# Kernel tuning notes

Measured on AMD Instinct MI355X. Metric: run time of the kernel, lower is better.

## Reference

```python
import jax, jax.numpy as jnp
import numpy as np

D_MODEL = 1024
NUM_HEAD = 16


def setup_inputs() -> dict:
    key = jax.random.key(0)
    ks = jax.random.split(key, 11)
    B, S, D = 2, 2048, D_MODEL
    scale = 1.0 / np.sqrt(D)
    inp = {
        "Q": jax.random.normal(ks[0], (B, S, D), jnp.float32),
        "K": jax.random.normal(ks[1], (B, S, D), jnp.float32),
        "V": jax.random.normal(ks[2], (B, S, D), jnp.float32),
        "Wq": jax.random.normal(ks[3], (D, D), jnp.float32) * scale,
        "bq": jax.random.normal(ks[4], (D,), jnp.float32) * 0.01,
        "Wk": jax.random.normal(ks[5], (D, D), jnp.float32) * scale,
        "bk": jax.random.normal(ks[6], (D,), jnp.float32) * 0.01,
        "Wv": jax.random.normal(ks[7], (D, D), jnp.float32) * scale,
        "bv": jax.random.normal(ks[8], (D,), jnp.float32) * 0.01,
        "Wo": jax.random.normal(ks[9], (D, D), jnp.float32) * scale,
        "bo": jax.random.normal(ks[10], (D,), jnp.float32) * 0.01,
    }
    return inp


def reference(Q, K, V, Wq, bq, Wk, bk, Wv, bv, Wo, bo):
    b, vc, d_model = Q.shape
    h = NUM_HEAD
    hd = d_model // h
    # projections (torch Linear: x @ W.T + b)
    q = (Q @ Wq.T + bq).reshape(b, vc, h, hd)
    k = (K @ Wk.T + bk).reshape(b, vc, h, hd)
    v = (V @ Wv.T + bv).reshape(b, vc, h, hd)
    # scores [b,h,q,k]
    atten = jnp.einsum('bqhd,bkhd->bhqk', q, k) / np.sqrt(hd).astype(jnp.float32)
    atten = jax.nn.softmax(atten, axis=3)
    # weighted values -> [b,q,h,hd]
    out = jnp.einsum('bhqd,bdhv->bqhv', atten, v).reshape(b, vc, d_model)
    return out @ Wo.T + bo
```

## Files before the change

### kernel.cpp

```cpp
#include <hip/hip_runtime.h>

#define S_LEN 2048
#define DM 1024
#define NH 16
#define HD 64
#define NB 2

typedef unsigned short u16;
typedef __attribute__((ext_vector_type(8))) short s16x8;
typedef __attribute__((ext_vector_type(8))) unsigned short u16x8;
typedef __attribute__((ext_vector_type(4))) float fx4;
typedef __attribute__((ext_vector_type(2))) unsigned u32x2;

__device__ __forceinline__ u16 f2bf(float f) {
  unsigned u = __builtin_bit_cast(unsigned, f);
  return (u16)((u + 0x7FFFu + ((u >> 16) & 1u)) >> 16);
}

__device__ __forceinline__ unsigned cvt_pk_bf16(float a, float b) {
  unsigned r;
  asm("v_cvt_pk_bf16_f32 %0, %1, %2" : "=v"(r) : "v"(a), "v"(b));
  return r;
}

__device__ __forceinline__ void gload16(const void* g, void* l) {
  __builtin_amdgcn_global_load_lds(
      (const __attribute__((address_space(1))) unsigned*)g,
      (__attribute__((address_space(3))) unsigned*)l, 16, 0, 0);
}

__device__ __forceinline__ fx4 mfma16(s16x8 a, s16x8 b, fx4 c) {
  return __builtin_amdgcn_mfma_f32_16x16x32_bf16(a, b, c, 0, 0, 0);
}

__global__ __launch_bounds__(256) void cvt_all_kernel(
    const float* __restrict__ Q, const float* __restrict__ K,
    const float* __restrict__ V, const float* __restrict__ Wq,
    const float* __restrict__ Wk, const float* __restrict__ Wv,
    const float* __restrict__ Wo, u16* __restrict__ Qc, u16* __restrict__ Kc,
    u16* __restrict__ Vc, u16* __restrict__ Wqb, u16* __restrict__ Wkb,
    u16* __restrict__ Wvb, u16* __restrict__ Wob) {
  const int blk = blockIdx.x;
  const float* src;
  u16* dst;
  float scale = 1.0f;
  int off;
  if (blk < 2048)      { src = Q;  dst = Qc;  off = blk; }
  else if (blk < 4096) { src = K;  dst = Kc;  off = blk - 2048; }
  else if (blk < 6144) { src = V;  dst = Vc;  off = blk - 4096; }
  else if (blk < 6656) { src = Wq; dst = Wqb; off = blk - 6144; scale = 0.18033688f; }
  else if (blk < 7168) { src = Wk; dst = Wkb; off = blk - 6656; }
  else if (blk < 7680) { src = Wv; dst = Wvb; off = blk - 7168; }
  else                 { src = Wo; dst = Wob; off = blk - 7680; }
  const int i = (off * 256 + (int)threadIdx.x) * 8;
  fx4 a = *(const fx4*)(src + i);
  fx4 b = *(const fx4*)(src + i + 4);
  u16x8 o;
  o[0] = f2bf(a[0] * scale); o[1] = f2bf(a[1] * scale);
  o[2] = f2bf(a[2] * scale); o[3] = f2bf(a[3] * scale);
  o[4] = f2bf(b[0] * scale); o[5] = f2bf(b[1] * scale);
  o[6] = f2bf(b[2] * scale); o[7] = f2bf(b[3] * scale);
  *(u16x8*)(dst + i) = o;
}

__device__ __forceinline__ void store_out(u16* C, size_t idx, float v) { C[idx] = f2bf(v); }
__device__ __forceinline__ void store_out(float* C, size_t idx, float v) { C[idx] = v; }

template <typename OUT>
__device__ __forceinline__ void gemm_db_body(const u16* __restrict__ A,
                                             const u16* __restrict__ Bt,
                                             const float* __restrict__ bias,
                                             float bscale, OUT* __restrict__ C,
                                             int m0, int n0) {
  __shared__ u16 Al[2][128 * 32];
  __shared__ u16 Bl[2][128 * 32];
  const int tid = threadIdx.x;
  const int wid = tid >> 6, lane = tid & 63;
  const int g = lane >> 4, lr = lane & 15;
  const int wr = wid >> 1, wc = wid & 1;
  const int row0 = tid >> 2, ch = tid & 3;
  const int chx = ch ^ ((row0 >> 1) & 3);

  fx4 acc[4][4] = {};

  auto stage = [&](int buf, int k0) {
    gload16(A + (size_t)(m0 + row0) * 1024 + k0 + chx * 8,
            (char*)Al[buf] + wid * 1024);
    gload16(A + (size_t)(m0 + 64 + row0) * 1024 + k0 + chx * 8,
            (char*)Al[buf] + 4096 + wid * 1024);
    gload16(Bt + (size_t)(n0 + row0) * 1024 + k0 + chx * 8,
            (char*)Bl[buf] + wid * 1024);
    gload16(Bt + (size_t)(n0 + 64 + row0) * 1024 + k0 + chx * 8,
            (char*)Bl[buf] + 4096 + wid * 1024);
  };
  auto compute = [&](int cur) {
    s16x8 a[4], b[4];
#pragma unroll
    for (int m = 0; m < 4; ++m) {
      const int row = wr * 64 + m * 16 + lr;
      a[m] = *(const s16x8*)((char*)Al[cur] + row * 64 + (g ^ ((row >> 1) & 3)) * 16);
    }
#pragma unroll
    for (int n = 0; n < 4; ++n) {
      const int row = wc * 64 + n * 16 + lr;
      b[n] = *(const s16x8*)((char*)Bl[cur] + row * 64 + (g ^ ((row >> 1) & 3)) * 16);
    }
    __builtin_amdgcn_s_setprio(1);
#pragma unroll
    for (int m = 0; m < 4; ++m)
#pragma unroll
      for (int n = 0; n < 4; ++n) acc[m][n] = mfma16(a[m], b[n], acc[m][n]);
    __builtin_amdgcn_s_setprio(0);
  };

  stage(0, 0);
  __syncthreads();

#pragma unroll 1
  for (int t = 0; t < 32; t += 2) {
    stage(1, (t + 1) * 32);
    compute(0);
    __syncthreads();
    if (t + 2 < 32) stage(0, (t + 2) * 32);
    compute(1);
    __syncthreads();
  }

#pragma unroll
  for (int n = 0; n < 4; ++n) {
    const int col = n0 + wc * 64 + n * 16 + lr;
    const float bv = bias[col] * bscale;
#pragma unroll
    for (int m = 0; m < 4; ++m) {
      const int row = m0 + wr * 64 + m * 16 + g * 4;
#pragma unroll
      for (int j = 0; j < 4; ++j)
        store_out(C, (size_t)(row + j) * 1024 + col, acc[m][n][j] + bv);
    }
  }
}

__global__ __launch_bounds__(256, 3) void gemm_qkv_kernel(
    const u16* Qc, const u16* Kc, const u16* Vc, const u16* Wq, const u16* Wk,
    const u16* Wv, const float* bq, const float* bk, const float* bv, u16* q,
    u16* k, u16* v) {
  const int hw = blockIdx.x + (blockIdx.y << 3) + (blockIdx.z << 8);
  const int xcd = hw & 7, j = hw >> 3;
  const int x = j & 7;
  const int p = xcd + ((j >> 3) << 3);
  const int y = p & 31, z = p >> 5;

  const u16* A;
  const u16* B;
  const float* bias;
  u16* C;
  float bs;
  if (z == 0)      { A = Qc; B = Wq; bias = bq; C = q; bs = 0.18033688f; }
  else if (z == 1) { A = Kc; B = Wk; bias = bk; C = k; bs = 1.0f; }
  else             { A = Vc; B = Wv; bias = bv; C = v; bs = 1.0f; }
  gemm_db_body<u16>(A, B, bias, bs, C, y * 128, x * 128);
}

__global__ __launch_bounds__(256, 3) void gemm_out_kernel(const u16* ctx,
                                                          const u16* Wo,
                                                          const float* bo,
                                                          float* out) {
  const int hw = blockIdx.x + (blockIdx.y << 3);
  const int xcd = hw & 7, j = hw >> 3;
  const int x = j & 7;
  const int y = xcd + ((j >> 3) << 3);
  gemm_db_body<float>(ctx, Wo, bo, 1.0f, out, y * 128, x * 128);
}

__global__ __launch_bounds__(256) void transpose_v_kernel(const u16* __restrict__ v,
                                                          u16* __restrict__ vt) {
  const int bh = blockIdx.y;
  const int b = bh >> 4, h = bh & 15;
  const int s0 = blockIdx.x * 32;
  const int d = threadIdx.x & 63;
  const int c = threadIdx.x >> 6;
  const int s = s0 + c * 8;
  const u16* src = v + ((size_t)(b * S_LEN + s)) * DM + h * HD + d;
  u16x8 o;
#pragma unroll
  for (int e = 0; e < 8; ++e) o[e] = src[(size_t)e * DM];
  *(u16x8*)(vt + ((size_t)(bh * 64 + d)) * S_LEN + s) = o;
}

__global__ __launch_bounds__(256, 4) void attn_kernel(const u16* __restrict__ qb,
                                                      const u16* __restrict__ kb,
                                                      const u16* __restrict__ vt,
                                                      u16* __restrict__ ctx) {
  __shared__ u16 Kl[2][64 * 64];
  __shared__ u16 Vl[2][64 * 64];
  __shared__ u16 Pl[4][16 * 64];

  const int tid = threadIdx.x, wid = tid >> 6, lane = tid & 63;
  const int g = lane >> 4, lr = lane & 15;
  const int rswz = (lr & 7) * 8;
  const int pswz = (lr & 7) * 16;
  char* Pb = (char*)&Pl[wid][0];

  const int hw = blockIdx.x;
  const int xcd = hw & 7, slot = hw >> 3;
  const int bh = xcd * 4 + (slot >> 5);
  const int b = bh >> 4, h = bh & 15;
  const int q0 = (slot & 31) * 64;

  const u16* qp = qb + ((size_t)(b * S_LEN + q0 + wid * 16 + lr)) * DM + h * HD;
  s16x8 aq[2];
  aq[0] = *(const s16x8*)(qp + g * 8);
  aq[1] = *(const s16x8*)(qp + 32 + g * 8);

  fx4 accO[4] = {};
  float lrun = 0.f;

  const int srow = tid >> 3, sch = tid & 7;
  const int schx = sch ^ (srow & 7);
  const u16* kbase = kb + ((size_t)b * S_LEN) * DM + h * HD;
  const u16* vtbase = vt + ((size_t)bh * 64) * S_LEN;

#define STAGE(buf, kv)                                                             \
  do {                                                                             \
    gload16(kbase + (size_t)((kv) + srow) * DM + schx * 8,                         \
            (char*)Kl[buf] + wid * 1024);                                          \
    gload16(kbase + (size_t)((kv) + 32 + srow) * DM + schx * 8,                    \
            (char*)Kl[buf] + 4096 + wid * 1024);                                   \
    gload16(vtbase + (size_t)srow * S_LEN + (kv) + schx * 8,                       \
            (char*)Vl[buf] + wid * 1024);                                          \
    gload16(vtbase + (size_t)(32 + srow) * S_LEN + (kv) + schx * 8,                \
            (char*)Vl[buf] + 4096 + wid * 1024);                                   \
  } while (0)

  auto compute_tile = [&](const u16* Kc0, const u16* Vc0) {
    fx4 s[4] = {};
    __builtin_amdgcn_s_setprio(1);
#pragma unroll
    for (int ks = 0; ks < 2; ++ks) {
#pragma unroll
      for (int c = 0; c < 4; ++c) {
        s16x8 kf =
            *(const s16x8*)(Kc0 + (c * 16 + lr) * 64 + ((ks * 32 + g * 8) ^ rswz));
        s[c] = mfma16(kf, aq[ks], s[c]);
      }
    }
    __builtin_amdgcn_s_setprio(0);

#pragma unroll
    for (int c = 0; c < 4; ++c)
#pragma unroll
      for (int j = 0; j < 4; ++j) s[c][j] = __builtin_amdgcn_exp2f(s[c][j]);
    {
      const float r0 = (s[0][0] + s[0][1]) + (s[0][2] + s[0][3]);
      const float r1 = (s[1][0] + s[1][1]) + (s[1][2] + s[1][3]);
      const float r2 = (s[2][0] + s[2][1]) + (s[2][2] + s[2][3]);
      const float r3 = (s[3][0] + s[3][1]) + (s[3][2] + s[3][3]);
      lrun += (r0 + r1) + (r2 + r3);
    }

#pragma unroll
    for (int c = 0; c < 4; ++c) {
      u32x2 w;
      w[0] = cvt_pk_bf16(s[c][0], s[c][1]);
      w[1] = cvt_pk_bf16(s[c][2], s[c][3]);
      *(u32x2*)(Pb + lr * 128 + ((c * 32 + g * 8) ^ pswz)) = w;
    }

    __builtin_amdgcn_s_setprio(1);
#pragma unroll
    for (int ks = 0; ks < 2; ++ks) {
      s16x8 pb = *(const s16x8*)(Pb + lr * 128 + ((ks * 64 + g * 16) ^ pswz));
#pragma unroll
      for (int c = 0; c < 4; ++c) {
        s16x8 vf =
            *(const s16x8*)(Vc0 + (c * 16 + lr) * 64 + ((ks * 32 + g * 8) ^ rswz));
        accO[c] = mfma16(vf, pb, accO[c]);
      }
    }
    __builtin_amdgcn_s_setprio(0);
  };

  STAGE(0, 0);
  __syncthreads();

  for (int t = 0; t < 32; t += 2) {
    if (t + 1 < 32) STAGE(1, (t + 1) * 64);
    compute_tile(Kl[0], Vl[0]);
    __syncthreads();
    if (t + 2 < 32) STAGE(0, (t + 2) * 64);
    compute_tile(Kl[1], Vl[1]);
    __syncthreads();
  }
#undef STAGE

  lrun += __shfl_xor(lrun, 16);
  lrun += __shfl_xor(lrun, 32);
  const float inv = 1.0f / lrun;
  u16* op = ctx + ((size_t)(b * S_LEN + q0 + wid * 16 + lr)) * DM + h * HD;
#pragma unroll
  for (int c = 0; c < 4; ++c) {
    u32x2 w;
    w[0] = cvt_pk_bf16(accO[c][0] * inv, accO[c][1] * inv);
    w[1] = cvt_pk_bf16(accO[c][2] * inv, accO[c][3] * inv);
    *(u32x2*)(op + c * 16 + g * 4) = w;
  }
}

extern "C" void kernel_launch(void* const* d_in, const int* in_sizes, int n_in,
                              void* d_out, int out_size, void* d_ws, size_t ws_size,
                              hipStream_t stream) {
  const float* Q = (const float*)d_in[0];
  const float* K = (const float*)d_in[1];
  const float* V = (const float*)d_in[2];
  const float* Wq = (const float*)d_in[3];
  const float* bq = (const float*)d_in[4];
  const float* Wk = (const float*)d_in[5];
  const float* bk = (const float*)d_in[6];
  const float* Wv = (const float*)d_in[7];
  const float* bv = (const float*)d_in[8];
  const float* Wo = (const float*)d_in[9];
  const float* bo = (const float*)d_in[10];
  float* out = (float*)d_out;

  char* ws = (char*)d_ws;
  const size_t SZ_T = (size_t)NB * S_LEN * DM * 2;
  const size_t SZ_W = (size_t)DM * DM * 2;

  u16* Wqb = (u16*)(ws);
  u16* Wkb = (u16*)(ws + SZ_W);
  u16* Wvb = (u16*)(ws + 2 * SZ_W);
  u16* Wob = (u16*)(ws + 3 * SZ_W);
  u16* Qc  = (u16*)(ws + 4 * SZ_W);
  u16* Kc  = (u16*)(ws + 4 * SZ_W + SZ_T);
  u16* Vc  = (u16*)(ws + 4 * SZ_W + 2 * SZ_T);
  u16* qb  = (u16*)(ws + 4 * SZ_W + 3 * SZ_T);
  u16* kb  = (u16*)(ws + 4 * SZ_W + 4 * SZ_T);
  u16* vb  = (u16*)(ws + 4 * SZ_W + 5 * SZ_T);
  u16* vtb = Qc;
  u16* ctx = Kc;

  cvt_all_kernel<<<8192, 256, 0, stream>>>(Q, K, V, Wq, Wk, Wv, Wo, Qc, Kc, Vc,
                                           Wqb, Wkb, Wvb, Wob);

  gemm_qkv_kernel<<<dim3(8, 32, 3), 256, 0, stream>>>(Qc, Kc, Vc, Wqb, Wkb, Wvb,
                                                      bq, bk, bv, qb, kb, vb);

  transpose_v_kernel<<<dim3(64, 32), 256, 0, stream>>>(vb, vtb);

  attn_kernel<<<1024, 256, 0, stream>>>(qb, kb, vtb, ctx);

  gemm_out_kernel<<<dim3(8, 32), 256, 0, stream>>>(ctx, Wob, bo, out);
}
```

Measured before the change: 130.1 us.

## Triple-buffer GEMM pipeline and fuse V transpose into QKV projection epilogue

The shared GEMM body moves from double to triple-buffered LDS staging, keeping two tiles of loads in flight and using explicit vmcnt waits and barriers in place of full __syncthreads. The V projection epilogue now writes bf16 results directly in the transposed [b,h,d,s] layout, so the separate transpose kernel and its extra read/write pass over V are gone. The costs are more LDS per block, which may reduce occupancy, and scattered 8-byte stores in the V epilogue.

New measurement: 119.3 us. 8.3% less time.

```diff
diff --git a/kernel.cpp b/kernel.cpp
--- a/kernel.cpp
+++ b/kernel.cpp
@@ -67,13 +67,14 @@
 __device__ __forceinline__ void store_out(float* C, size_t idx, float v) { C[idx] = v; }
 
 template <typename OUT>
-__device__ __forceinline__ void gemm_db_body(const u16* __restrict__ A,
-                                             const u16* __restrict__ Bt,
-                                             const float* __restrict__ bias,
-                                             float bscale, OUT* __restrict__ C,
-                                             int m0, int n0) {
-  __shared__ u16 Al[2][128 * 32];
-  __shared__ u16 Bl[2][128 * 32];
+__device__ __forceinline__ void gemm_pipe_body(const u16* __restrict__ A,
+                                               const u16* __restrict__ Bt,
+                                               const float* __restrict__ bias,
+                                               float bscale, OUT* __restrict__ C,
+                                               u16* __restrict__ vt, bool vout,
+                                               int m0, int n0) {
+  __shared__ u16 Al[3][128 * 32];
+  __shared__ u16 Bl[3][128 * 32];
   const int tid = threadIdx.x;
   const int wid = tid >> 6, lane = tid & 63;
   const int g = lane >> 4, lr = lane & 15;
@@ -83,28 +84,27 @@
 
   fx4 acc[4][4] = {};
 
-  auto stage = [&](int buf, int k0) {
-    gload16(A + (size_t)(m0 + row0) * 1024 + k0 + chx * 8,
-            (char*)Al[buf] + wid * 1024);
+  auto stage = [&](u16* Ab, u16* Bb, int k0) {
+    gload16(A + (size_t)(m0 + row0) * 1024 + k0 + chx * 8, (char*)Ab + wid * 1024);
     gload16(A + (size_t)(m0 + 64 + row0) * 1024 + k0 + chx * 8,
-            (char*)Al[buf] + 4096 + wid * 1024);
-    gload16(Bt + (size_t)(n0 + row0) * 1024 + k0 + chx * 8,
-            (char*)Bl[buf] + wid * 1024);
+            (char*)Ab + 4096 + wid * 1024);
+    gload16(Bt + (size_t)(n0 + row0) * 1024 + k0 + chx * 8, (char*)Bb + wid * 1024);
     gload16(Bt + (size_t)(n0 + 64 + row0) * 1024 + k0 + chx * 8,
-            (char*)Bl[buf] + 4096 + wid * 1024);
+            (char*)Bb + 4096 + wid * 1024);
   };
-  auto compute = [&](int cur) {
-    s16x8 a[4], b[4];
+  auto readfrag = [&](const u16* Ab, const u16* Bb, s16x8* a, s16x8* b) {
 #pragma unroll
     for (int m = 0; m < 4; ++m) {
       const int row = wr * 64 + m * 16 + lr;
-      a[m] = *(const s16x8*)((char*)Al[cur] + row * 64 + (g ^ ((row >> 1) & 3)) * 16);
+      a[m] = *(const s16x8*)((const char*)Ab + row * 64 + (g ^ ((row >> 1) & 3)) * 16);
     }
 #pragma unroll
     for (int n = 0; n < 4; ++n) {
       const int row = wc * 64 + n * 16 + lr;
-      b[n] = *(const s16x8*)((char*)Bl[cur] + row * 64 + (g ^ ((row >> 1) & 3)) * 16);
-    }
+      b[n] = *(const s16x8*)((const char*)Bb + row * 64 + (g ^ ((row >> 1) & 3)) * 16);
+    }
+  };
+  auto domfma = [&](s16x8* a, s16x8* b) {
     __builtin_amdgcn_s_setprio(1);
 #pragma unroll
     for (int m = 0; m < 4; ++m)
@@ -113,29 +113,63 @@
     __builtin_amdgcn_s_setprio(0);
   };
 
-  stage(0, 0);
-  __syncthreads();
+#define GSTEP(BUF, T, NW)                                                     \
+  do {                                                                        \
+    asm volatile("s_waitcnt vmcnt(" #NW ")" ::: "memory");                    \
+    __builtin_amdgcn_s_barrier();                                             \
+    __builtin_amdgcn_sched_barrier(0);                                        \
+    s16x8 afr[4], bfr[4];                                                     \
+    readfrag(Al[BUF], Bl[BUF], afr, bfr);                                     \
+    asm volatile("s_waitcnt lgkmcnt(0)" ::: "memory");                        \
+    __builtin_amdgcn_sched_barrier(0);                                        \
+    __builtin_amdgcn_s_barrier();                                             \
+    __builtin_amdgcn_sched_barrier(0);                                        \
+    if ((T) + 3 < 32) stage(Al[BUF], Bl[BUF], ((T) + 3) * 32);                \
+    domfma(afr, bfr);                                                         \
+  } while (0)
+
+  stage(Al[0], Bl[0], 0);
+  stage(Al[1], Bl[1], 32);
+  stage(Al[2], Bl[2], 64);
 
 #pragma unroll 1
-  for (int t = 0; t < 32; t += 2) {
-    stage(1, (t + 1) * 32);
-    compute(0);
-    __syncthreads();
-    if (t + 2 < 32) stage(0, (t + 2) * 32);
-    compute(1);
-    __syncthreads();
+  for (int t = 0; t < 30; t += 3) {
+    GSTEP(0, t, 8);
+    GSTEP(1, t + 1, 8);
+    GSTEP(2, t + 2, 8);
   }
-
-#pragma unroll
-  for (int n = 0; n < 4; ++n) {
-    const int col = n0 + wc * 64 + n * 16 + lr;
-    const float bv = bias[col] * bscale;
-#pragma unroll
-    for (int m = 0; m < 4; ++m) {
-      const int row = m0 + wr * 64 + m * 16 + g * 4;
-#pragma unroll
-      for (int j = 0; j < 4; ++j)
-        store_out(C, (size_t)(row + j) * 1024 + col, acc[m][n][j] + bv);
+  GSTEP(0, 30, 4);
+  GSTEP(1, 31, 0);
+#undef GSTEP
+
+  if (vout) {
+#pragma unroll
+    for (int n = 0; n < 4; ++n) {
+      const int col = n0 + wc * 64 + n * 16 + lr;
+      const float bv = bias[col] * bscale;
+      const int h = col >> 6, d = col & 63;
+#pragma unroll
+      for (int m = 0; m < 4; ++m) {
+        const int row = m0 + wr * 64 + m * 16 + g * 4;
+        const int bb = row >> 11, s = row & 2047;
+        u32x2 w;
+        w[0] = cvt_pk_bf16(acc[m][n][0] + bv, acc[m][n][1] + bv);
+        w[1] = cvt_pk_bf16(acc[m][n][2] + bv, acc[m][n][3] + bv);
+        *(u32x2*)(vt + ((size_t)(((bb << 4) | h) * 64 + d)) * 2048 + s) = w;
+      }
+    }
+  } else {
+#pragma unroll
+    for (int n = 0; n < 4; ++n) {
+      const int col = n0 + wc * 64 + n * 16 + lr;
+      const float bv = bias[col] * bscale;
+#pragma unroll
+      for (int m = 0; m < 4; ++m) {
+        const int row = m0 + wr * 64 + m * 16 + g * 4;
+#pragma unroll
+        for (int j = 0; j < 4; ++j)
+          store_out(C, (size_t)(row + j) * 1024 + col, acc[m][n][j] + bv);
+      }
     }
   }
 }
@@ -143,22 +177,22 @@
 __global__ __launch_bounds__(256, 3) void gemm_qkv_kernel(
     const u16* Qc, const u16* Kc, const u16* Vc, const u16* Wq, const u16* Wk,
     const u16* Wv, const float* bq, const float* bk, const float* bv, u16* q,
-    u16* k, u16* v) {
+    u16* k, u16* vt) {
   const int hw = blockIdx.x + (blockIdx.y << 3) + (blockIdx.z << 8);
   const int xcd = hw & 7, j = hw >> 3;
   const int x = j & 7;
   const int p = xcd + ((j >> 3) << 3);
   const int y = p & 31, z = p >> 5;
 
-  const u16* A;
-  const u16* B;
-  const float* bias;
-  u16* C;
-  float bs;
-  if (z == 0)      { A = Qc; B = Wq; bias = bq; C = q; bs = 0.18033688f; }
-  else if (z == 1) { A = Kc; B = Wk; bias = bk; C = k; bs = 1.0f; }
-  else             { A = Vc; B = Wv; bias = bv; C = v; bs = 1.0f; }
-  gemm_db_body<u16>(A, B, bias, bs, C, y * 128, x * 128);
+  const u16 *Ap, *Bp;
+  const float* bp;
+  u16* Cp;
+  float bs = 1.0f;
+  bool vo = false;
+  if (z == 0)      { Ap = Qc; Bp = Wq; bp = bq; Cp = q; bs = 0.18033688f; }
+  else if (z == 1) { Ap = Kc; Bp = Wk; bp = bk; Cp = k; }
+  else             { Ap = Vc; Bp = Wv; bp = bv; Cp = q; vo = true; }
+  gemm_pipe_body<u16>(Ap, Bp, bp, bs, Cp, vt, vo, y * 128, x * 128);
 }
 
 __global__ __launch_bounds__(256, 3) void gemm_out_kernel(const u16* ctx,
@@ -169,22 +203,7 @@
   const int xcd = hw & 7, j = hw >> 3;
   const int x = j & 7;
   const int y = xcd + ((j >> 3) << 3);
-  gemm_db_body<float>(ctx, Wo, bo, 1.0f, out, y * 128, x * 128);
-}
-
-__global__ __launch_bounds__(256) void transpose_v_kernel(const u16* __restrict__ v,
-                                                          u16* __restrict__ vt) {
-  const int bh = blockIdx.y;
-  const int b = bh >> 4, h = bh & 15;
-  const int s0 = blockIdx.x * 32;
-  const int d = threadIdx.x & 63;
-  const int c = threadIdx.x >> 6;
-  const int s = s0 + c * 8;
-  const u16* src = v + ((size_t)(b * S_LEN + s)) * DM + h * HD + d;
-  u16x8 o;
-#pragma unroll
-  for (int e = 0; e < 8; ++e) o[e] = src[(size_t)e * DM];
-  *(u16x8*)(vt + ((size_t)(bh * 64 + d)) * S_LEN + s) = o;
+  gemm_pipe_body<float>(ctx, Wo, bo, 1.0f, out, nullptr, false, y * 128, x * 128);
 }
 
 __global__ __launch_bounds__(256, 4) void attn_kernel(const u16* __restrict__ qb,
@@ -335,17 +354,14 @@
   u16* Vc  = (u16*)(ws + 4 * SZ_W + 2 * SZ_T);
   u16* qb  = (u16*)(ws + 4 * SZ_W + 3 * SZ_T);
   u16* kb  = (u16*)(ws + 4 * SZ_W + 4 * SZ_T);
-  u16* vb  = (u16*)(ws + 4 * SZ_W + 5 * SZ_T);
-  u16* vtb = Qc;
-  u16* ctx = Kc;
+  u16* vtb = (u16*)(ws + 4 * SZ_W + 5 * SZ_T);
+  u16* ctx = Qc;
 
   cvt_all_kernel<<<8192, 256, 0, stream>>>(Q, K, V, Wq, Wk, Wv, Wo, Qc, Kc, Vc,
                                            Wqb, Wkb, Wvb, Wob);
 
   gemm_qkv_kernel<<<dim3(8, 32, 3), 256, 0, stream>>>(Qc, Kc, Vc, Wqb, Wkb, Wvb,
-                                                      bq, bk, bv, qb, kb, vb);
-
-  transpose_v_kernel<<<dim3(64, 32), 256, 0, stream>>>(vb, vtb);
+                                                      bq, bk, bv, qb, kb, vtb);
 
   attn_kernel<<<1024, 256, 0, stream>>>(qb, kb, vtb, ctx);
 
```
